# Performance work log

Hardware: AMD Instinct MI355X
Metric: run time of the kernel (lower is better)

## Reference

```python
import jax, jax.numpy as jnp
import numpy as np

D_MODEL = 2048
D_STATE = 128
D_CONV = 4
EXPAND = 2
HEADDIM = 64
NGROUPS = 1
D_INNER = EXPAND * D_MODEL            # 4096
NHEADS = D_INNER // HEADDIM           # 64
D_XBC = D_INNER + 2 * NGROUPS * D_STATE   # 4352
D_IN_PROJ = 2 * D_INNER + 2 * NGROUPS * D_STATE + NHEADS  # 8512
BLOCK_LEN = 64


def _segsum(x):
    # x: (..., T) -> (..., T, T) with segsum[i, j] = sum_{j < k <= i} x[k], -inf above diag
    T = x.shape[-1]
    xc = jnp.cumsum(x, axis=-1)
    seg = xc[..., :, None] - xc[..., None, :]
    mask = jnp.tril(jnp.ones((T, T), dtype=bool))
    return jnp.where(mask, seg, -jnp.inf)


def _ssd_scan(X, A, B, C, block_len):
    # X: (b, L, h, p), A: (b, L, h), B/C: (b, L, h, n)
    b, L, h, p = X.shape
    c = L // block_len
    X = X.reshape(b, c, block_len, h, p)
    A = A.reshape(b, c, block_len, h).transpose(0, 3, 1, 2)  # b h c l
    B = B.reshape(b, c, block_len, h, -1)
    C = C.reshape(b, c, block_len, h, -1)
    A_cumsum = jnp.cumsum(A, axis=-1)                         # b h c l
    Lmat = jnp.exp(_segsum(A))                                # b h c l l
    Y_diag = jnp.einsum('bclhn,bcshn,bhcls,bcshp->bclhp', C, B, Lmat, X)
    decay_states = jnp.exp(A_cumsum[:, :, :, -1:] - A_cumsum)  # b h c l
    states = jnp.einsum('bclhn,bhcl,bclhp->bchpn', B, decay_states, X)
    init = jnp.zeros_like(states[:, :1])
    states = jnp.concatenate([init, states], axis=1)          # b (c+1) h p n
    A_last = jnp.pad(A_cumsum[:, :, :, -1], ((0, 0), (0, 0), (1, 0)))  # b h (c+1)
    decay_chunk = jnp.exp(_segsum(A_last))                    # b h (c+1) (c+1)
    new_states = jnp.einsum('bhzc,bchpn->bzhpn', decay_chunk, states)
    states = new_states[:, 1:]                                # b c h p n
    state_decay_out = jnp.exp(A_cumsum)                       # b h c l
    Y_off = jnp.einsum('bclhn,bchpn,bhcl->bclhp', C, states, state_decay_out)
    return (Y_diag + Y_off).reshape(b, L, h, p)


def _forward(x, in_proj_w, conv_w, conv_b, A_log, D, dt_bias, norm_w, out_proj_w):
    Bsz, L, _ = x.shape
    proj = x @ in_proj_w.T                                    # (B, L, d_in_proj)
    z = proj[:, :, :D_INNER]
    xBC = proj[:, :, D_INNER:D_INNER + D_XBC]
    dt_raw = proj[:, :, D_INNER + D_XBC:]
    # depthwise causal conv1d (torch pads both sides then truncates to L == left pad only)
    xBC_t = xBC.transpose(0, 2, 1)                            # (B, C, L)
    conv = jax.lax.conv_general_dilated(
        xBC_t, conv_w, window_strides=(1,), padding=[(D_CONV - 1, 0)],
        feature_group_count=D_XBC, dimension_numbers=('NCH', 'OIH', 'NCH'))
    conv = conv + conv_b[None, :, None]
    xBC = jax.nn.silu(conv).transpose(0, 2, 1)                # (B, L, d_xBC)
    x_ssm = xBC[:, :, :D_INNER]
    B_param = xBC[:, :, D_INNER:D_INNER + NGROUPS * D_STATE]
    C_param = xBC[:, :, D_INNER + NGROUPS * D_STATE:]
    dt = jax.nn.softplus(dt_raw + dt_bias)                    # (B, L, nheads)
    A = -jnp.exp(A_log)                                       # (nheads,)
    x_heads = x_ssm.reshape(Bsz, L, NHEADS, HEADDIM)
    hpg = NHEADS // NGROUPS
    X = x_heads * dt[..., None]
    A_disc = dt * A[None, None, :]
    B_heads = jnp.repeat(B_param.reshape(Bsz, L, NGROUPS, D_STATE), hpg, axis=2)
    C_heads = jnp.repeat(C_param.reshape(Bsz, L, NGROUPS, D_STATE), hpg, axis=2)
    pad_len = (BLOCK_LEN - L % BLOCK_LEN) % BLOCK_LEN
    if pad_len > 0:
        X = jnp.pad(X, ((0, 0), (0, pad_len), (0, 0), (0, 0)))
        A_disc = jnp.pad(A_disc, ((0, 0), (0, pad_len), (0, 0)))
        B_heads = jnp.pad(B_heads, ((0, 0), (0, pad_len), (0, 0), (0, 0)))
        C_heads = jnp.pad(C_heads, ((0, 0), (0, pad_len), (0, 0), (0, 0)))
    Y = _ssd_scan(X, A_disc, B_heads, C_heads, BLOCK_LEN)[:, :L]
    Y = Y + x_heads * D[None, None, :, None]
    y = Y.reshape(Bsz, L, D_INNER)
    y = y * jax.nn.silu(z)
    rms = jnp.sqrt(jnp.mean(y * y, axis=-1, keepdims=True) + 1e-5)
    y = y / rms * norm_w
    return y @ out_proj_w.T


def setup_inputs() -> dict:
    key = jax.random.key(0)
    ks = jax.random.split(key, 8)
    x = jax.random.normal(ks[0], (2, 2048, D_MODEL), dtype=jnp.float32)
    in_proj_w = jax.random.normal(ks[1], (D_IN_PROJ, D_MODEL), dtype=jnp.float32) * 0.02
    conv_w = jax.random.normal(ks[2], (D_XBC, 1, D_CONV), dtype=jnp.float32) * 0.2
    conv_b = jnp.zeros((D_XBC,), dtype=jnp.float32)
    A_log = jnp.log(jnp.arange(1, NHEADS + 1, dtype=jnp.float32))
    D = jnp.ones((NHEADS,), dtype=jnp.float32)
    dt_bias = jax.random.normal(ks[3], (NHEADS,), dtype=jnp.float32) * 0.1
    norm_w = jnp.ones((D_INNER,), dtype=jnp.float32)
    out_proj_w = jax.random.normal(ks[4], (D_MODEL, D_INNER), dtype=jnp.float32) * 0.02
    return {"x": x, "in_proj_w": in_proj_w, "conv_w": conv_w, "conv_b": conv_b,
            "A_log": A_log, "D": D, "dt_bias": dt_bias, "norm_w": norm_w,
            "out_proj_w": out_proj_w}


def reference(x, in_proj_w, conv_w, conv_b, A_log, D, dt_bias, norm_w, out_proj_w):
    return _forward(x, in_proj_w, conv_w, conv_b, A_log, D, dt_bias, norm_w, out_proj_w)
```

## Files before the change

### kernel.cpp

```cpp
#include <hip/hip_runtime.h>
#include <cstddef>
#include <cstdint>

#define B_SZ    2
#define SEQ     2048
#define DMODEL  2048
#define DINNER  4096
#define DSTATE  128
#define NHEADS  64
#define HEADDIM 64
#define DXBC    4352
#define NPROJ   8448
#define CHUNK   64
#define NCHUNK  32
#define TOKENS  (B_SZ*SEQ)

typedef __attribute__((ext_vector_type(8))) short short8;
typedef __attribute__((ext_vector_type(4))) float floatx4;

__device__ inline float us2f(unsigned short u) {
  union { uint32_t i; float f; } c; c.i = ((uint32_t)u) << 16; return c.f;
}
__device__ inline unsigned short f2us(float f) {
  union { float f; uint32_t i; } c; c.f = f;
  uint32_t r = (c.i + 0x7fffu + ((c.i >> 16) & 1u)) >> 16;
  return (unsigned short)r;
}
__device__ inline float plo(uint32_t v) {
  union { uint32_t i; float f; } c; c.i = v << 16; return c.f;
}
__device__ inline float phi(uint32_t v) {
  union { uint32_t i; float f; } c; c.i = v & 0xffff0000u; return c.f;
}

__global__ __launch_bounds__(256) void cast_f32_bf16(
    const float* __restrict__ src, unsigned short* __restrict__ dst, int n) {
  int i = (blockIdx.x * 256 + threadIdx.x) * 4;
  if (i < n) {
    float4 v = *(const float4*)(src + i);
    ushort4 o;
    o.x = f2us(v.x); o.y = f2us(v.y); o.z = f2us(v.z); o.w = f2us(v.w);
    *(ushort4*)(dst + i) = o;
  }
}

template<int OUT_BF16>
__global__ __launch_bounds__(256, 2) void gemm_bt_p3(
    const unsigned short* __restrict__ A, const unsigned short* __restrict__ B,
    void* __restrict__ Cout, int M, int N, int K, int GM) {
  __shared__ __align__(16) unsigned short sT[3 * 12288];
  const int tid  = threadIdx.x;
  const int lane = tid & 63;
  const int wc   = tid >> 6;
  const int fr   = lane & 15;
  const int fq   = lane >> 4;

  const int nwg  = gridDim.x;
  int wgid = blockIdx.x;
  if ((nwg & 7) == 0) wgid = (wgid & 7) * (nwg >> 3) + (wgid >> 3);
  const int bm = (wgid % GM) * 128;
  const int bn = (wgid / GM) * 256;

  floatx4 acc[8][4];
  #pragma unroll
  for (int i = 0; i < 8; ++i)
    #pragma unroll
    for (int j = 0; j < 4; ++j) acc[i][j] = (floatx4){0.f, 0.f, 0.f, 0.f};

  auto stage = [&](int rb, int kb) {
    unsigned short* dst = (unsigned short*)sT + rb * 12288;
    #pragma unroll
    for (int q = 0; q < 6; ++q) {
      if (q < 2) {
        int i = q * 256 + tid;
        int row = i >> 2, slot = i & 3;
        const unsigned short* g =
            A + (size_t)(bm + row) * K + kb + 8 * (slot ^ ((row >> 1) & 3));
        __builtin_amdgcn_global_load_lds(
            (const __attribute__((address_space(1))) uint32_t*)g,
            (__attribute__((address_space(3))) uint32_t*)(dst + i * 8), 16, 0, 0);
      } else {
        int i = (q - 2) * 256 + tid;
        int row = i >> 2, slot = i & 3;
        const unsigned short* g =
            B + (size_t)(bn + row) * K + kb + 8 * (slot ^ ((row >> 1) & 3));
        __builtin_amdgcn_global_load_lds(
            (const __attribute__((address_space(1))) uint32_t*)g,
            (__attribute__((address_space(3))) uint32_t*)(dst + 4096 + i * 8), 16, 0, 0);
      }
    }
  };

  const int NH = K >> 5;
  stage(0, 0);
  stage(1, 32);
  asm volatile("s_waitcnt vmcnt(6)" ::: "memory");
  asm volatile("s_barrier" ::: "memory");

  int cb = 0, sb = 2;
  for (int h = 0; h < NH; ++h) {
    const unsigned short* buf = (const unsigned short*)sT + cb * 12288;
    if (h + 2 < NH) stage(sb, (h + 2) << 5);

    short8 af[8], bf[4];
    #pragma unroll
    for (int i = 0; i < 8; ++i) {
      int row = i * 16 + fr;
      af[i] = *(const short8*)(buf + row * 32 + 8 * (fq ^ ((row >> 1) & 3)));
    }
    #pragma unroll
    for (int j = 0; j < 4; ++j) {
      int row = wc * 64 + j * 16 + fr;
      bf[j] = *(const short8*)(buf + 4096 + row * 32 + 8 * (fq ^ ((row >> 1) & 3)));
    }
    __builtin_amdgcn_s_setprio(1);
    #pragma unroll
    for (int i = 0; i < 8; ++i)
      #pragma unroll
      for (int j = 0; j < 4; ++j)
        acc[i][j] = __builtin_amdgcn_mfma_f32_16x16x32_bf16(af[i], bf[j], acc[i][j], 0, 0, 0);
    __builtin_amdgcn_s_setprio(0);

    if (h < NH - 2) asm volatile("s_waitcnt vmcnt(6) lgkmcnt(0)" ::: "memory");
    else            asm volatile("s_waitcnt vmcnt(0) lgkmcnt(0)" ::: "memory");
    asm volatile("s_barrier" ::: "memory");
    cb = (cb == 2) ? 0 : cb + 1;
    sb = (sb == 2) ? 0 : sb + 1;
  }

  #pragma unroll
  for (int i = 0; i < 8; ++i) {
    #pragma unroll
    for (int j = 0; j < 4; ++j) {
      int col = bn + wc * 64 + j * 16 + fr;
      #pragma unroll
      for (int r = 0; r < 4; ++r) {
        int row = bm + i * 16 + fq * 4 + r;
        if (OUT_BF16)
          ((unsigned short*)Cout)[(size_t)row * N + col] = f2us(acc[i][j][r]);
        else
          ((float*)Cout)[(size_t)row * N + col] = acc[i][j][r];
      }
    }
  }
}

__device__ inline void loadA4(const float* p, float* d) {
  float4 v = *(const float4*)p; d[0]=v.x; d[1]=v.y; d[2]=v.z; d[3]=v.w;
}
__device__ inline void loadA4(const unsigned short* p, float* d) {
  ushort4 v = *(const ushort4*)p;
  d[0]=us2f(v.x); d[1]=us2f(v.y); d[2]=us2f(v.z); d[3]=us2f(v.w);
}
__device__ inline void store8(float* C, size_t off, const float* v) {
  *(float4*)(C + off)     = make_float4(v[0], v[1], v[2], v[3]);
  *(float4*)(C + off + 4) = make_float4(v[4], v[5], v[6], v[7]);
}
__device__ inline void store8(unsigned short* C, size_t off, const float* v) {
  ushort4 a; a.x=f2us(v[0]); a.y=f2us(v[1]); a.z=f2us(v[2]); a.w=f2us(v[3]);
  ushort4 b; b.x=f2us(v[4]); b.y=f2us(v[5]); b.z=f2us(v[6]); b.w=f2us(v[7]);
  *(ushort4*)(C + off) = a; *(ushort4*)(C + off + 4) = b;
}

template<typename AT, typename OT>
__global__ __launch_bounds__(256) void gemm_nt(
    const AT* __restrict__ A, const float* __restrict__ Bw,
    OT* __restrict__ C, int M, int N, int K) {
  __shared__ float As[16][128+4];
  __shared__ float Bs[16][128+4];
  const int bm = blockIdx.y * 128;
  const int bn = blockIdx.x * 128;
  const int tid = threadIdx.x;
  const int tx = tid & 15, ty = tid >> 4;

  float acc[8][8];
  #pragma unroll
  for (int i = 0; i < 8; ++i)
    #pragma unroll
    for (int j = 0; j < 8; ++j) acc[i][j] = 0.f;

  for (int k0 = 0; k0 < K; k0 += 16) {
    #pragma unroll
    for (int r = 0; r < 2; ++r) {
      int i = tid + r * 256;
      int m  = i >> 2;
      int kv = (i & 3) << 2;
      float va[4];
      loadA4(A + (size_t)(bm + m) * K + k0 + kv, va);
      As[kv+0][m] = va[0]; As[kv+1][m] = va[1]; As[kv+2][m] = va[2]; As[kv+3][m] = va[3];
      float vb[4] = {0.f, 0.f, 0.f, 0.f};
      if (bn + m < N) loadA4(Bw + (size_t)(bn + m) * K + k0 + kv, vb);
      Bs[kv+0][m] = vb[0]; Bs[kv+1][m] = vb[1]; Bs[kv+2][m] = vb[2]; Bs[kv+3][m] = vb[3];
    }
    __syncthreads();
    #pragma unroll
    for (int kk = 0; kk < 16; ++kk) {
      float ra[8], rb[8];
      *(float4*)&ra[0] = *(const float4*)&As[kk][ty*8];
      *(float4*)&ra[4] = *(const float4*)&As[kk][ty*8+4];
      *(float4*)&rb[0] = *(const float4*)&Bs[kk][tx*8];
      *(float4*)&rb[4] = *(const float4*)&Bs[kk][tx*8+4];
      #pragma unroll
      for (int i = 0; i < 8; ++i)
        #pragma unroll
        for (int j = 0; j < 8; ++j) acc[i][j] += ra[i] * rb[j];
    }
    __syncthreads();
  }
  #pragma unroll
  for (int i = 0; i < 8; ++i) {
    int m  = bm + ty*8 + i;
    int n0 = bn + tx*8;
    if (n0 < N) store8(C, (size_t)m * N + n0, &acc[i][0]);
  }
}

__global__ __launch_bounds__(256) void dt_gemm(
    const float* __restrict__ x, const float* __restrict__ W,
    float* __restrict__ dtr) {
  __shared__ float sX[32][64];
  __shared__ float sW[32][64];
  const int tid = threadIdx.x;
  const int t0 = blockIdx.x * 64;
  const int tx = tid & 15;
  const int ty = tid >> 4;
  const float* Wdt = W + (size_t)NPROJ * DMODEL;

  float acc[4][4];
  #pragma unroll
  for (int i = 0; i < 4; ++i)
    #pragma unroll
    for (int j = 0; j < 4; ++j) acc[i][j] = 0.f;

  const int r  = tid >> 3;
  const int kq = (tid & 7) * 4;

  for (int k0 = 0; k0 < DMODEL; k0 += 32) {
    __syncthreads();
    #pragma unroll
    for (int rr = 0; rr < 2; ++rr) {
      int t = r + rr * 32;
      float4 v = *(const float4*)(x + (size_t)(t0 + t) * DMODEL + k0 + kq);
      sX[kq+0][t] = v.x; sX[kq+1][t] = v.y; sX[kq+2][t] = v.z; sX[kq+3][t] = v.w;
    }
    #pragma unroll
    for (int rr = 0; rr < 2; ++rr) {
      int hh = r + rr * 32;
      float4 v = *(const float4*)(Wdt + (size_t)hh * DMODEL + k0 + kq);
      sW[kq+0][hh] = v.x; sW[kq+1][hh] = v.y; sW[kq+2][hh] = v.z; sW[kq+3][hh] = v.w;
    }
    __syncthreads();
    #pragma unroll
    for (int kk = 0; kk < 32; ++kk) {
      float4 ra = *(const float4*)&sX[kk][ty*4];
      float4 rb = *(const float4*)&sW[kk][tx*4];
      float a[4] = {ra.x, ra.y, ra.z, ra.w};
      float b[4] = {rb.x, rb.y, rb.z, rb.w};
      #pragma unroll
      for (int i = 0; i < 4; ++i)
        #pragma unroll
        for (int j = 0; j < 4; ++j)
          acc[i][j] += a[i] * b[j];
    }
  }
  #pragma unroll
  for (int i = 0; i < 4; ++i) {
    float4 o = make_float4(acc[i][0], acc[i][1], acc[i][2], acc[i][3]);
    *(float4*)(dtr + (size_t)(t0 + ty*4 + i) * NHEADS + tx*4) = o;
  }
}

__global__ __launch_bounds__(256) void bc_conv_g(
    const unsigned short* __restrict__ proj, const float* __restrict__ cw,
    const float* __restrict__ cb, unsigned short* __restrict__ bcact,
    float* __restrict__ gbuf) {
  const int c = blockIdx.x & 31;
  const int b = blockIdx.x >> 5;
  const int tid = threadIdx.x;
  const int t0 = b * SEQ + c * CHUNK;
  __shared__ unsigned short sB[64*130];
  __shared__ unsigned short sC[64*130];
  for (int i = tid; i < 64*256; i += 256) {
    int s = i >> 8, ch = i & 255;
    int cx = 4096 + ch;
    int lb = c * CHUNK + s;
    float acc = cb[cx];
    #pragma unroll
    for (int j = 0; j < 4; ++j) {
      int ll = lb - 3 + j;
      if (ll >= 0)
        acc += cw[cx*4 + j] * us2f(proj[(size_t)(b*SEQ + ll) * NPROJ + DINNER + cx]);
    }
    float v = acc / (1.f + expf(-acc));
    unsigned short uv = f2us(v);
    if (ch < 128) sB[s*130 + ch] = uv;
    else          sC[s*130 + (ch - 128)] = uv;
    bcact[(size_t)(t0 + s) * 256 + ch] = uv;
  }
  __syncthreads();
  const int l = tid >> 2, q = tid & 3;
  float g[16];
  #pragma unroll
  for (int j = 0; j < 16; ++j) g[j] = 0.f;
  const uint32_t* Cu = (const uint32_t*)&sC[l * 130];
  for (int u = 0; u < 64; ++u) {
    uint32_t cv = Cu[u];
    float c0 = plo(cv), c1 = phi(cv);
    #pragma unroll
    for (int j = 0; j < 16; ++j) {
      uint32_t bv = ((const uint32_t*)&sB[(q*16 + j) * 130])[u];
      g[j] += c0 * plo(bv) + c1 * phi(bv);
    }
  }
  float* gr = gbuf + ((size_t)(b*NCHUNK + c)) * 4096 + l*64 + q*16;
  #pragma unroll
  for (int j = 0; j < 16; ++j) gr[j] = g[j];
}

__global__ __launch_bounds__(256, 4) void ssd_phase_a2_mfma(
    const unsigned short* __restrict__ proj, const unsigned short* __restrict__ bcact,
    const float* __restrict__ dtr, const float* __restrict__ cw,
    const float* __restrict__ cb, const float* __restrict__ A_log,
    const float* __restrict__ dt_bias, const float* __restrict__ gbuf,
    const float* __restrict__ Dv,
    unsigned short* __restrict__ cs, float* __restrict__ acs,
    unsigned short* __restrict__ yscan) {
  const int h = blockIdx.x & 63;
  const int c = (blockIdx.x >> 6) & 31;
  const int b = blockIdx.x >> 11;
  const int tid = threadIdx.x;
  const int t0 = b * SEQ + c * CHUNK;
  const int lane = tid & 63, wave = tid >> 6;
  const int fr = lane & 15, fq = lane >> 4;

  __shared__ __align__(16) unsigned short sBt[128*72];
  __shared__ __align__(16) unsigned short sXh[64*72];
  __shared__ __align__(16) unsigned short sW[64*72];
  __shared__ float sdt[64], sAc[64], sdecay[64];

  const float Ah = -expf(A_log[h]);
  if (tid < 64) {
    float raw = dtr[(size_t)(t0 + tid) * NHEADS + h] + dt_bias[h];
    float dt = (raw > 20.f) ? raw : log1pf(expf(raw));
    sdt[tid] = dt;
    float v = dt * Ah;
    #pragma unroll
    for (int off = 1; off < 64; off <<= 1) {
      float o = __shfl_up(v, off, 64);
      if (tid >= off) v += o;
    }
    sAc[tid] = v;
    float alast = __shfl(v, 63, 64);
    sdecay[tid] = expf(alast - v);
    acs[((size_t)((b*NHEADS + h)*NCHUNK + c))*64 + tid] = v;
  }
  __syncthreads();
  for (int i = tid; i < 64*128; i += 256) {
    int s = i >> 7, n = i & 127;
    float v = us2f(bcact[(size_t)(t0 + s) * 256 + n]) * sdt[s] * sdecay[s];
    sBt[n*72 + s] = f2us(v);
  }
  for (int i = tid; i < 64*64; i += 256) {
    int s = i >> 6, p = i & 63;
    int cx = h * HEADDIM + p;
    int lb = c * CHUNK + s;
    float acc = cb[cx];
    #pragma unroll
    for (int j = 0; j < 4; ++j) {
      int ll = lb - 3 + j;
      if (ll >= 0)
        acc += cw[cx*4 + j] * us2f(proj[(size_t)(b*SEQ + ll) * NPROJ + DINNER + cx]);
    }
    float xh = acc / (1.f + expf(-acc));
    sXh[p*72 + s] = f2us(xh);
  }
  {
    const float* gr = gbuf + ((size_t)(b*NCHUNK + c)) * 4096;
    for (int i = tid; i < 4096; i += 256) {
      int l = i >> 6, s = i & 63;
      float w = (s <= l) ? gr[i] * expf(sAc[l] - sAc[s]) * sdt[s] : 0.f;
      sW[l*72 + s] = f2us(w);
    }
  }
  __syncthreads();

  floatx4 accy[4];
  #pragma unroll
  for (int j = 0; j < 4; ++j) accy[j] = (floatx4){0.f, 0.f, 0.f, 0.f};
  #pragma unroll
  for (int k0 = 0; k0 < 64; k0 += 32) {
    short8 af = *(const short8*)(sW + (wave*16 + fr)*72 + k0 + fq*8);
    #pragma unroll
    for (int j = 0; j < 4; ++j) {
      short8 bf = *(const short8*)(sXh + (j*16 + fr)*72 + k0 + fq*8);
      accy[j] = __builtin_amdgcn_mfma_f32_16x16x32_bf16(af, bf, accy[j], 0, 0, 0);
    }
  }
  const float Dh = Dv[h];
  #pragma unroll
  for (int j = 0; j < 4; ++j) {
    int p = j*16 + fr;
    #pragma unroll
    for (int r = 0; r < 4; ++r) {
      int l = wave*16 + fq*4 + r;
      float yd = accy[j][r] + us2f(sXh[p*72 + l]) * Dh;
      yscan[(size_t)(t0 + l) * DINNER + h*HEADDIM + p] = f2us(yd);
    }
  }
  floatx4 accs[8];
  #pragma unroll
  for (int j = 0; j < 8; ++j) accs[j] = (floatx4){0.f, 0.f, 0.f, 0.f};
  #pragma unroll
  for (int k0 = 0; k0 < 64; k0 += 32) {
    short8 af = *(const short8*)(sXh + (wave*16 + fr)*72 + k0 + fq*8);
    #pragma unroll
    for (int j = 0; j < 8; ++j) {
      short8 bf = *(const short8*)(sBt + (j*16 + fr)*72 + k0 + fq*8);
      accs[j] = __builtin_amdgcn_mfma_f32_16x16x32_bf16(af, bf, accs[j], 0, 0, 0);
    }
  }
  const size_t csb = ((size_t)((b*NHEADS + h)*NCHUNK + c)) * (HEADDIM*DSTATE);
  #pragma unroll
  for (int j = 0; j < 8; ++j) {
    int n = j*16 + fr;
    #pragma unroll
    for (int r = 0; r < 4; ++r) {
      int p = wave*16 + fq*4 + r;
      cs[csb + p*128 + n] = f2us(accs[j][r]);
    }
  }
}

__global__ __launch_bounds__(256) void ssd_scan_states(
    unsigned short* __restrict__ cs, const float* __restrict__ acs) {
  int idx = blockIdx.x * 256 + threadIdx.x;
  int e  = idx & 8191;
  int bh = idx >> 13;
  float S = 0.f;
  for (int c = 0; c < NCHUNK; ++c) {
    float al = acs[((size_t)bh*NCHUNK + c)*64 + 63];
    size_t o = ((size_t)bh*NCHUNK + c)*(HEADDIM*DSTATE) + e;
    S = S * expf(al) + us2f(cs[o]);
    cs[o] = f2us(S);
  }
}

__global__ __launch_bounds__(256, 4) void ssd_phase_c_mfma(
    const unsigned short* __restrict__ bcact, const unsigned short* __restrict__ cs,
    const float* __restrict__ acs, unsigned short* __restrict__ yscan) {
  const int h = blockIdx.x & 63;
  const int c = (blockIdx.x >> 6) & 31;
  const int b = blockIdx.x >> 11;
  const int tid = threadIdx.x;
  const int t0 = b * SEQ + c * CHUNK;
  const int lane = tid & 63, wave = tid >> 6;
  const int fr = lane & 15, fq = lane >> 4;

  __shared__ __align__(16) unsigned short sC[64*136];
  __shared__ __align__(16) unsigned short sS[64*136];
  __shared__ float seAc[64];

  const size_t csb = ((size_t)((b*NHEADS + h)*NCHUNK + c)) * (HEADDIM*DSTATE);
  for (int i = tid; i < 8192; i += 256) {
    int p = i >> 7, n = i & 127;
    sS[p*136 + n] = cs[csb + i];
  }
  for (int i = tid; i < 8192; i += 256) {
    int l = i >> 7, n = i & 127;
    sC[l*136 + n] = bcact[(size_t)(t0 + l) * 256 + 128 + n];
  }
  if (tid < 64) seAc[tid] = expf(acs[((size_t)((b*NHEADS + h)*NCHUNK + c))*64 + tid]);
  __syncthreads();

  floatx4 acc[4];
  #pragma unroll
  for (int j = 0; j < 4; ++j) acc[j] = (floatx4){0.f, 0.f, 0.f, 0.f};
  #pragma unroll
  for (int k0 = 0; k0 < 128; k0 += 32) {
    short8 af = *(const short8*)(sC + (wave*16 + fr)*136 + k0 + fq*8);
    #pragma unroll
    for (int j = 0; j < 4; ++j) {
      short8 bf = *(const short8*)(sS + (j*16 + fr)*136 + k0 + fq*8);
      acc[j] = __builtin_amdgcn_mfma_f32_16x16x32_bf16(af, bf, acc[j], 0, 0, 0);
    }
  }
  #pragma unroll
  for (int j = 0; j < 4; ++j) {
    int p = j*16 + fr;
    #pragma unroll
    for (int r = 0; r < 4; ++r) {
      int l = wave*16 + fq*4 + r;
      size_t yi = (size_t)(t0 + l) * DINNER + h*HEADDIM + p;
      yscan[yi] = f2us(us2f(yscan[yi]) + acc[j][r] * seAc[l]);
    }
  }
}

__global__ __launch_bounds__(256) void gate_rmsnorm2(
    const unsigned short* __restrict__ proj, const float* __restrict__ norm_w,
    unsigned short* __restrict__ yscan) {
  const int t = blockIdx.x;
  const int tid = threadIdx.x;
  __shared__ float ybuf[DINNER];
  __shared__ float wpart[4];
  __shared__ float sinv;
  float ss = 0.f;
  for (int i = tid; i < DINNER; i += 256) {
    float zv = us2f(proj[(size_t)t * NPROJ + i]);
    float yv = us2f(yscan[(size_t)t * DINNER + i]) * (zv / (1.f + expf(-zv)));
    ybuf[i] = yv;
    ss += yv * yv;
  }
  #pragma unroll
  for (int off = 32; off > 0; off >>= 1) ss += __shfl_down(ss, off, 64);
  if ((tid & 63) == 0) wpart[tid >> 6] = ss;
  __syncthreads();
  if (tid == 0) {
    float tot = wpart[0] + wpart[1] + wpart[2] + wpart[3];
    sinv = 1.f / sqrtf(tot / (float)DINNER + 1e-5f);
  }
  __syncthreads();
  float inv = sinv;
  for (int i = tid; i < DINNER; i += 256)
    yscan[(size_t)t * DINNER + i] = f2us(ybuf[i] * inv * norm_w[i]);
}

__global__ __launch_bounds__(512) void ssd_fused(
    const unsigned short* __restrict__ proj, const float* __restrict__ dtr,
    const float* __restrict__ cw, const float* __restrict__ cb,
    const float* __restrict__ A_log, const float* __restrict__ dt_bias,
    unsigned short* __restrict__ yscan) {
  const int h = blockIdx.x & 63;
  const int b = blockIdx.x >> 6;
  const int tid = threadIdx.x;

  __shared__ unsigned short sB[64*130];
  __shared__ unsigned short sC[64*130];
  __shared__ unsigned short sX[64*66];
  __shared__ float sW[64*65];
  __shared__ float sdt[64], sAc[64], sdecay[64], seAc[64];

  const float Ah = -expf(A_log[h]);
  const float dbias = dt_bias[h];

  float S[16];
  #pragma unroll
  for (int j = 0; j < 16; ++j) S[j] = 0.f;

  const int lG  = tid >> 3;
  const int oc  = tid & 7;

  for (int c = 0; c < NCHUNK; ++c) {
    const int t0 = b * SEQ + c * CHUNK;
    __syncthreads();
    if (tid < 64) {
      float raw = dtr[(size_t)(t0 + tid) * NHEADS + h] + dbias;
      sdt[tid] = (raw > 20.f) ? raw : log1pf(expf(raw));
    }
    for (int i = tid; i < 64*256; i += 512) {
      int s = i >> 8, ch = i & 255;
      int cx = 4096 + ch;
      int lb = c * CHUNK + s;
      float acc = cb[cx];
      #pragma unroll
      for (int j = 0; j < 4; ++j) {
        int ll = lb - 3 + j;
        if (ll >= 0)
          acc += cw[cx*4 + j] * us2f(proj[(size_t)(b*SEQ + ll) * NPROJ + DINNER + cx]);
      }
      float v = acc / (1.f + expf(-acc));
      if (ch < 128) sB[s*130 + ch] = f2us(v);
      else          sC[s*130 + (ch - 128)] = f2us(v);
    }
    __syncthreads();
    if (tid == 0) {
      float run = 0.f;
      for (int s = 0; s < CHUNK; ++s) { run += sdt[s] * Ah; sAc[s] = run; }
    }
    __syncthreads();
    if (tid < 64) {
      float last = sAc[63];
      sdecay[tid] = expf(last - sAc[tid]);
      seAc[tid]   = expf(sAc[tid]);
    }
    for (int i = tid; i < 64*64; i += 512) {
      int s = i >> 6, p = i & 63;
      int cx = h * HEADDIM + p;
      int lb = c * CHUNK + s;
      float acc = cb[cx];
      #pragma unroll
      for (int j = 0; j < 4; ++j) {
        int ll = lb - 3 + j;
        if (ll >= 0)
          acc += cw[cx*4 + j] * us2f(proj[(size_t)(b*SEQ + ll) * NPROJ + DINNER + cx]);
      }
      float v = acc / (1.f + expf(-acc));
      sX[s*66 + p] = f2us(v * sdt[s]);
    }
    __syncthreads();

    float g[8];
    #pragma unroll
    for (int j = 0; j < 8; ++j) g[j] = 0.f;
    {
      const uint32_t* Cu = (const uint32_t*)&sC[lG * 130];
      for (int u = 0; u < 64; ++u) {
        uint32_t cv = Cu[u];
        float c0 = plo(cv), c1 = phi(cv);
        #pragma unroll
        for (int j = 0; j < 8; ++j) {
          uint32_t bv = ((const uint32_t*)&sB[(oc*8 + j) * 130])[u];
          g[j] += c0 * plo(bv) + c1 * phi(bv);
        }
      }
    }
    {
      float acl = sAc[lG];
      #pragma unroll
      for (int j = 0; j < 8; ++j) {
        int s = oc*8 + j;
        sW[lG*65 + s] = (s <= lG) ? g[j] * expf(acl - sAc[s]) : 0.f;
      }
    }
    {
      float elast = expf(sAc[63]);
      #pragma unroll
      for (int j = 0; j < 16; ++j) S[j] *= elast;
      for (int s = 0; s < CHUNK; ++s) {
        float w = sdecay[s] * us2f(sX[s*66 + lG]);
        const uint32_t* Bu = (const uint32_t*)&sB[s*130 + oc*16];
        #pragma unroll
        for (int ju = 0; ju < 8; ++ju) {
          uint32_t bv = Bu[ju];
          S[2*ju]   += plo(bv) * w;
          S[2*ju+1] += phi(bv) * w;
        }
      }
    }
    __syncthreads();
    #pragma unroll
    for (int j = 0; j < 16; ++j) sB[lG*130 + oc*16 + j] = f2us(S[j]);
    __syncthreads();
    for (int o = tid; o < CHUNK*HEADDIM; o += 512) {
      int l = o >> 6, p = o & 63;
      float yd = 0.f;
      for (int s = 0; s <= l; ++s)
        yd += sW[l*65 + s] * us2f(sX[s*66 + p]);
      float yo = 0.f;
      const uint32_t* Cu = (const uint32_t*)&sC[l * 130];
      const uint32_t* Su = (const uint32_t*)&sB[p * 130];
      for (int u = 0; u < 64; ++u) {
        uint32_t cv = Cu[u], sv = Su[u];
        yo += plo(cv) * plo(sv) + phi(cv) * phi(sv);
      }
      float y = yd + yo * seAc[l];
      yscan[(size_t)(t0 + l) * DINNER + h * HEADDIM + p] = f2us(y);
    }
  }
}

__global__ __launch_bounds__(256) void gate_rmsnorm_dskip(
    const unsigned short* __restrict__ proj, const float* __restrict__ cw,
    const float* __restrict__ cb, const float* __restrict__ Dv,
    const float* __restrict__ norm_w, unsigned short* __restrict__ yscan) {
  const int t = blockIdx.x;
  const int tid = threadIdx.x;
  const int b = t >> 11, lb = t & 2047;
  __shared__ float ybuf[DINNER];
  __shared__ float wpart[4];
  __shared__ float sinv;
  float ss = 0.f;
  for (int i = tid; i < DINNER; i += 256) {
    float zv = us2f(proj[(size_t)t * NPROJ + i]);
    float acc = cb[i];
    #pragma unroll
    for (int j = 0; j < 4; ++j) {
      int ll = lb - 3 + j;
      if (ll >= 0)
        acc += cw[i*4 + j] * us2f(proj[(size_t)(b*SEQ + ll) * NPROJ + DINNER + i]);
    }
    float xh = acc / (1.f + expf(-acc));
    float yv = us2f(yscan[(size_t)t * DINNER + i]) + xh * Dv[i >> 6];
    yv = yv * (zv / (1.f + expf(-zv)));
    ybuf[i] = yv;
    ss += yv * yv;
  }
  #pragma unroll
  for (int off = 32; off > 0; off >>= 1) ss += __shfl_down(ss, off, 64);
  if ((tid & 63) == 0) wpart[tid >> 6] = ss;
  __syncthreads();
  if (tid == 0) {
    float tot = wpart[0] + wpart[1] + wpart[2] + wpart[3];
    sinv = 1.f / sqrtf(tot / (float)DINNER + 1e-5f);
  }
  __syncthreads();
  float inv = sinv;
  for (int i = tid; i < DINNER; i += 256)
    yscan[(size_t)t * DINNER + i] = f2us(ybuf[i] * inv * norm_w[i]);
}

extern "C" void kernel_launch(void* const* d_in, const int* in_sizes, int n_in,
                              void* d_out, int out_size, void* d_ws, size_t ws_size,
                              hipStream_t stream) {
  const float* x          = (const float*)d_in[0];
  const float* in_proj_w  = (const float*)d_in[1];
  const float* conv_w     = (const float*)d_in[2];
  const float* conv_b     = (const float*)d_in[3];
  const float* A_log      = (const float*)d_in[4];
  const float* Dv         = (const float*)d_in[5];
  const float* dt_bias    = (const float*)d_in[6];
  const float* norm_w     = (const float*)d_in[7];
  const float* out_proj_w = (const float*)d_in[8];
  float* out = (float*)d_out;

  unsigned short* proj  = (unsigned short*)d_ws;
  float*          dtr   = (float*)(proj + (size_t)TOKENS * NPROJ);
  unsigned short* yscan = (unsigned short*)(dtr + (size_t)TOKENS * NHEADS);
  unsigned short* cs    = yscan + (size_t)TOKENS * DINNER;
  float*          acs   = (float*)(cs + (size_t)B_SZ*NHEADS*NCHUNK*HEADDIM*DSTATE);
  unsigned short* bcact = (unsigned short*)(acs + (size_t)B_SZ*NHEADS*NCHUNK*64);
  float*          gbuf  = (float*)(bcact + (size_t)TOKENS*256);
  const size_t NEEDED = (size_t)((char*)(gbuf + (size_t)B_SZ*NCHUNK*4096) - (char*)d_ws);

  unsigned short* xb  = cs;
  unsigned short* wib = xb + (size_t)TOKENS * DMODEL;
  unsigned short* wob = proj;

  if (ws_size >= NEEDED) {
    cast_f32_bf16<<<(TOKENS*DMODEL)/1024, 256, 0, stream>>>(x, xb, TOKENS*DMODEL);
    cast_f32_bf16<<<((size_t)NPROJ*DMODEL)/1024, 256, 0, stream>>>(in_proj_w, wib, NPROJ*DMODEL);
    {
      int nwg = (TOKENS/128) * (NPROJ/256);
      gemm_bt_p3<1><<<nwg, 256, 0, stream>>>(xb, wib, proj, TOKENS, NPROJ, DMODEL, TOKENS/128);
    }
    dt_gemm<<<TOKENS/64, 256, 0, stream>>>(x, in_proj_w, dtr);
    bc_conv_g<<<B_SZ*NCHUNK, 256, 0, stream>>>(proj, conv_w, conv_b, bcact, gbuf);
    ssd_phase_a2_mfma<<<B_SZ*NCHUNK*NHEADS, 256, 0, stream>>>(
        proj, bcact, dtr, conv_w, conv_b, A_log, dt_bias, gbuf, Dv, cs, acs, yscan);
    ssd_scan_states<<<(B_SZ*NHEADS*HEADDIM*DSTATE)/256, 256, 0, stream>>>(cs, acs);
    ssd_phase_c_mfma<<<B_SZ*NCHUNK*NHEADS, 256, 0, stream>>>(bcact, cs, acs, yscan);
    gate_rmsnorm2<<<TOKENS, 256, 0, stream>>>(proj, norm_w, yscan);
    cast_f32_bf16<<<((size_t)DMODEL*DINNER)/1024, 256, 0, stream>>>(out_proj_w, wob, DMODEL*DINNER);
    {
      int nwg = (TOKENS/128) * (DMODEL/256);
      gemm_bt_p3<0><<<nwg, 256, 0, stream>>>(yscan, wob, out, TOKENS, DMODEL, DINNER, TOKENS/128);
    }
  } else {
    {
      dim3 grid(NPROJ/128, TOKENS/128);
      gemm_nt<float, unsigned short><<<grid, 256, 0, stream>>>(
          x, in_proj_w, proj, TOKENS, NPROJ, DMODEL);
    }
    dt_gemm<<<TOKENS/64, 256, 0, stream>>>(x, in_proj_w, dtr);
    ssd_fused<<<B_SZ*NHEADS, 512, 0, stream>>>(proj, dtr, conv_w, conv_b,
                                               A_log, dt_bias, yscan);
    gate_rmsnorm_dskip<<<TOKENS, 256, 0, stream>>>(proj, conv_w, conv_b, Dv, norm_w, yscan);
    {
      dim3 grid(DMODEL/128, TOKENS/128);
      gemm_nt<unsigned short, float><<<grid, 256, 0, stream>>>(
          yscan, out_proj_w, out, TOKENS, DMODEL, DINNER);
    }
  }
}
```

Before: 796.0 us.

## Vectorize SSD helper kernels and use 64-row tiles for out-projection GEMM

Templates the bf16 GEMM on the M tile size and runs the out-projection with 64-row tiles, doubling the workgroup count for the small N=2048 GEMM. The conv, scan, chunk and gate/rmsnorm kernels now stage conv inputs in LDS, read them once, and use 16-byte vector loads and stores instead of scalar ones. The state scan now has each thread handle eight elements. Phase A's occupancy hint is lowered from 4 to 3 blocks to fit the extra LDS. These changes target memory inefficiency and low parallelism in the auxiliary kernels, at the cost of more LDS use and register pressure.

```diff
diff --git a/kernel.cpp b/kernel.cpp
--- a/kernel.cpp
+++ b/kernel.cpp
@@ -44,11 +44,16 @@
   }
 }
 
-template<int OUT_BF16>
+template<int OUT_BF16, int BMT>
 __global__ __launch_bounds__(256, 2) void gemm_bt_p3(
     const unsigned short* __restrict__ A, const unsigned short* __restrict__ B,
     void* __restrict__ Cout, int M, int N, int K, int GM) {
-  __shared__ __align__(16) unsigned short sT[3 * 12288];
+  constexpr int ACH   = BMT / 64;
+  constexpr int NCH   = ACH + 4;
+  constexpr int ABASE = ACH * 2048;
+  constexpr int BUFS  = (BMT + 256) * 32;
+  constexpr int NI    = BMT / 16;
+  __shared__ __align__(16) unsigned short sT[3 * BUFS];
   const int tid  = threadIdx.x;
   const int lane = tid & 63;
   const int wc   = tid >> 6;
@@ -58,20 +63,20 @@
   const int nwg  = gridDim.x;
   int wgid = blockIdx.x;
   if ((nwg & 7) == 0) wgid = (wgid & 7) * (nwg >> 3) + (wgid >> 3);
-  const int bm = (wgid % GM) * 128;
+  const int bm = (wgid % GM) * BMT;
   const int bn = (wgid / GM) * 256;
 
-  floatx4 acc[8][4];
-  #pragma unroll
-  for (int i = 0; i < 8; ++i)
+  floatx4 acc[NI][4];
+  #pragma unroll
+  for (int i = 0; i < NI; ++i)
     #pragma unroll
     for (int j = 0; j < 4; ++j) acc[i][j] = (floatx4){0.f, 0.f, 0.f, 0.f};
 
   auto stage = [&](int rb, int kb) {
-    unsigned short* dst = (unsigned short*)sT + rb * 12288;
-    #pragma unroll
-    for (int q = 0; q < 6; ++q) {
-      if (q < 2) {
+    unsigned short* dst = (unsigned short*)sT + rb * BUFS;
+    #pragma unroll
+    for (int q = 0; q < NCH; ++q) {
+      if (q < ACH) {
         int i = q * 256 + tid;
         int row = i >> 2, slot = i & 3;
         const unsigned short* g =
@@ -80,13 +85,13 @@
             (const __attribute__((address_space(1))) uint32_t*)g,
             (__attribute__((address_space(3))) uint32_t*)(dst + i * 8), 16, 0, 0);
       } else {
-        int i = (q - 2) * 256 + tid;
+        int i = (q - ACH) * 256 + tid;
         int row = i >> 2, slot = i & 3;
         const unsigned short* g =
             B + (size_t)(bn + row) * K + kb + 8 * (slot ^ ((row >> 1) & 3));
         __builtin_amdgcn_global_load_lds(
             (const __attribute__((address_space(1))) uint32_t*)g,
-            (__attribute__((address_space(3))) uint32_t*)(dst + 4096 + i * 8), 16, 0, 0);
+            (__attribute__((address_space(3))) uint32_t*)(dst + ABASE + i * 8), 16, 0, 0);
       }
     }
   };
@@ -94,42 +99,47 @@
   const int NH = K >> 5;
   stage(0, 0);
   stage(1, 32);
-  asm volatile("s_waitcnt vmcnt(6)" ::: "memory");
+  if constexpr (NCH == 6) asm volatile("s_waitcnt vmcnt(6)" ::: "memory");
+  else                    asm volatile("s_waitcnt vmcnt(5)" ::: "memory");
   asm volatile("s_barrier" ::: "memory");
 
   int cb = 0, sb = 2;
   for (int h = 0; h < NH; ++h) {
-    const unsigned short* buf = (const unsigned short*)sT + cb * 12288;
+    const unsigned short* buf = (const unsigned short*)sT + cb * BUFS;
     if (h + 2 < NH) stage(sb, (h + 2) << 5);
 
-    short8 af[8], bf[4];
-    #pragma unroll
-    for (int i = 0; i < 8; ++i) {
+    short8 af[NI], bf[4];
+    #pragma unroll
+    for (int i = 0; i < NI; ++i) {
       int row = i * 16 + fr;
       af[i] = *(const short8*)(buf + row * 32 + 8 * (fq ^ ((row >> 1) & 3)));
     }
     #pragma unroll
     for (int j = 0; j < 4; ++j) {
       int row = wc * 64 + j * 16 + fr;
-      bf[j] = *(const short8*)(buf + 4096 + row * 32 + 8 * (fq ^ ((row >> 1) & 3)));
+      bf[j] = *(const short8*)(buf + ABASE + row * 32 + 8 * (fq ^ ((row >> 1) & 3)));
     }
     __builtin_amdgcn_s_setprio(1);
     #pragma unroll
-    for (int i = 0; i < 8; ++i)
+    for (int i = 0; i < NI; ++i)
       #pragma unroll
       for (int j = 0; j < 4; ++j)
         acc[i][j] = __builtin_amdgcn_mfma_f32_16x16x32_bf16(af[i], bf[j], acc[i][j], 0, 0, 0);
     __builtin_amdgcn_s_setprio(0);
 
-    if (h < NH - 2) asm volatile("s_waitcnt vmcnt(6) lgkmcnt(0)" ::: "memory");
-    else            asm volatile("s_waitcnt vmcnt(0) lgkmcnt(0)" ::: "memory");
+    if (h < NH - 2) {
+      if constexpr (NCH == 6) asm volatile("s_waitcnt vmcnt(6) lgkmcnt(0)" ::: "memory");
+      else                    asm volatile("s_waitcnt vmcnt(5) lgkmcnt(0)" ::: "memory");
+    } else {
+      asm volatile("s_waitcnt vmcnt(0) lgkmcnt(0)" ::: "memory");
+    }
     asm volatile("s_barrier" ::: "memory");
     cb = (cb == 2) ? 0 : cb + 1;
     sb = (sb == 2) ? 0 : sb + 1;
   }
 
   #pragma unroll
-  for (int i = 0; i < 8; ++i) {
+  for (int i = 0; i < NI; ++i) {
     #pragma unroll
     for (int j = 0; j < 4; ++j) {
       int col = bn + wc * 64 + j * 16 + fr;
@@ -278,46 +288,70 @@
   const int b = blockIdx.x >> 5;
   const int tid = threadIdx.x;
   const int t0 = b * SEQ + c * CHUNK;
-  __shared__ unsigned short sB[64*130];
-  __shared__ unsigned short sC[64*130];
-  for (int i = tid; i < 64*256; i += 256) {
-    int s = i >> 8, ch = i & 255;
-    int cx = 4096 + ch;
-    int lb = c * CHUNK + s;
-    float acc = cb[cx];
-    #pragma unroll
-    for (int j = 0; j < 4; ++j) {
-      int ll = lb - 3 + j;
-      if (ll >= 0)
-        acc += cw[cx*4 + j] * us2f(proj[(size_t)(b*SEQ + ll) * NPROJ + DINNER + cx]);
-    }
-    float v = acc / (1.f + expf(-acc));
-    unsigned short uv = f2us(v);
-    if (ch < 128) sB[s*130 + ch] = uv;
-    else          sC[s*130 + (ch - 128)] = uv;
-    bcact[(size_t)(t0 + s) * 256 + ch] = uv;
+  __shared__ __align__(16) unsigned short sIn[67 * 256];
+  __shared__ __align__(16) unsigned short sB[64 * 136];
+  __shared__ __align__(16) unsigned short sC[64 * 136];
+  __shared__ float scw[256 * 4];
+  __shared__ float scb[256];
+
+  *(float4*)&scw[tid * 4] = *(const float4*)(cw + (size_t)(4096 + tid) * 4);
+  scb[tid] = cb[4096 + tid];
+
+  for (int i = tid; i < 67 * 32; i += 256) {
+    int r = i >> 5, ch0 = (i & 31) * 8;
+    int ll = c * CHUNK - 3 + r;
+    short8 v = {0,0,0,0,0,0,0,0};
+    if (ll >= 0)
+      v = *(const short8*)(proj + (size_t)(b * SEQ + ll) * NPROJ + 8192 + ch0);
+    *(short8*)&sIn[r * 256 + ch0] = v;
   }
   __syncthreads();
+
+  for (int i = tid; i < 64 * 32; i += 256) {
+    int s = i >> 5, ch0 = (i & 31) * 8;
+    short8 i0 = *(const short8*)&sIn[(s + 0) * 256 + ch0];
+    short8 i1 = *(const short8*)&sIn[(s + 1) * 256 + ch0];
+    short8 i2 = *(const short8*)&sIn[(s + 2) * 256 + ch0];
+    short8 i3 = *(const short8*)&sIn[(s + 3) * 256 + ch0];
+    short8 o;
+    #pragma unroll
+    for (int e = 0; e < 8; ++e) {
+      int ch = ch0 + e;
+      float a = scb[ch]
+        + scw[ch*4+0] * us2f((unsigned short)i0[e])
+        + scw[ch*4+1] * us2f((unsigned short)i1[e])
+        + scw[ch*4+2] * us2f((unsigned short)i2[e])
+        + scw[ch*4+3] * us2f((unsigned short)i3[e]);
+      float v = a / (1.f + expf(-a));
+      o[e] = (short)f2us(v);
+    }
+    if (ch0 < 128) *(short8*)&sB[s * 136 + ch0] = o;
+    else           *(short8*)&sC[s * 136 + (ch0 - 128)] = o;
+    *(short8*)(bcact + (size_t)(t0 + s) * 256 + ch0) = o;
+  }
+  __syncthreads();
+
   const int l = tid >> 2, q = tid & 3;
   float g[16];
   #pragma unroll
   for (int j = 0; j < 16; ++j) g[j] = 0.f;
-  const uint32_t* Cu = (const uint32_t*)&sC[l * 130];
+  const uint32_t* Cu = (const uint32_t*)&sC[l * 136];
   for (int u = 0; u < 64; ++u) {
     uint32_t cv = Cu[u];
     float c0 = plo(cv), c1 = phi(cv);
     #pragma unroll
     for (int j = 0; j < 16; ++j) {
-      uint32_t bv = ((const uint32_t*)&sB[(q*16 + j) * 130])[u];
+      uint32_t bv = ((const uint32_t*)&sB[(q*16 + j) * 136])[u];
       g[j] += c0 * plo(bv) + c1 * phi(bv);
     }
   }
   float* gr = gbuf + ((size_t)(b*NCHUNK + c)) * 4096 + l*64 + q*16;
   #pragma unroll
-  for (int j = 0; j < 16; ++j) gr[j] = g[j];
-}
-
-__global__ __launch_bounds__(256, 4) void ssd_phase_a2_mfma(
+  for (int j = 0; j < 4; ++j)
+    *(float4*)(gr + j*4) = make_float4(g[j*4], g[j*4+1], g[j*4+2], g[j*4+3]);
+}
+
+__global__ __launch_bounds__(256, 3) void ssd_phase_a2_mfma(
     const unsigned short* __restrict__ proj, const unsigned short* __restrict__ bcact,
     const float* __restrict__ dtr, const float* __restrict__ cw,
     const float* __restrict__ cb, const float* __restrict__ A_log,
@@ -333,9 +367,12 @@
   const int lane = tid & 63, wave = tid >> 6;
   const int fr = lane & 15, fq = lane >> 4;
 
+  __shared__ __align__(16) unsigned short sIn[67 * 64];
   __shared__ __align__(16) unsigned short sBt[128*72];
   __shared__ __align__(16) unsigned short sXh[64*72];
   __shared__ __align__(16) unsigned short sW[64*72];
+  __shared__ float cwl[64 * 4];
+  __shared__ float cbl[64];
   __shared__ float sdt[64], sAc[64], sdecay[64];
 
   const float Ah = -expf(A_log[h]);
@@ -354,32 +391,63 @@
     sdecay[tid] = expf(alast - v);
     acs[((size_t)((b*NHEADS + h)*NCHUNK + c))*64 + tid] = v;
   }
+  if (tid >= 64 && tid < 128) {
+    int p = tid - 64;
+    *(float4*)&cwl[p * 4] = *(const float4*)(cw + (size_t)(h * HEADDIM + p) * 4);
+    cbl[p] = cb[h * HEADDIM + p];
+  }
+  for (int i = tid; i < 67 * 8; i += 256) {
+    int r = i >> 3, p0 = (i & 7) * 8;
+    int ll = c * CHUNK - 3 + r;
+    short8 v = {0,0,0,0,0,0,0,0};
+    if (ll >= 0)
+      v = *(const short8*)(proj + (size_t)(b * SEQ + ll) * NPROJ + DINNER + h * HEADDIM + p0);
+    *(short8*)&sIn[r * 64 + p0] = v;
+  }
   __syncthreads();
-  for (int i = tid; i < 64*128; i += 256) {
-    int s = i >> 7, n = i & 127;
-    float v = us2f(bcact[(size_t)(t0 + s) * 256 + n]) * sdt[s] * sdecay[s];
-    sBt[n*72 + s] = f2us(v);
-  }
-  for (int i = tid; i < 64*64; i += 256) {
-    int s = i >> 6, p = i & 63;
-    int cx = h * HEADDIM + p;
-    int lb = c * CHUNK + s;
-    float acc = cb[cx];
-    #pragma unroll
-    for (int j = 0; j < 4; ++j) {
-      int ll = lb - 3 + j;
-      if (ll >= 0)
-        acc += cw[cx*4 + j] * us2f(proj[(size_t)(b*SEQ + ll) * NPROJ + DINNER + cx]);
-    }
-    float xh = acc / (1.f + expf(-acc));
-    sXh[p*72 + s] = f2us(xh);
+
+  for (int i = tid; i < 64 * 16; i += 256) {
+    int s = i >> 4, n0 = (i & 15) * 8;
+    float sc = sdt[s] * sdecay[s];
+    short8 v = *(const short8*)(bcact + (size_t)(t0 + s) * 256 + n0);
+    #pragma unroll
+    for (int e = 0; e < 8; ++e)
+      sBt[(n0 + e) * 72 + s] = f2us(us2f((unsigned short)v[e]) * sc);
+  }
+  for (int i = tid; i < 64 * 8; i += 256) {
+    int s = i >> 3, p0 = (i & 7) * 8;
+    short8 i0 = *(const short8*)&sIn[(s + 0) * 64 + p0];
+    short8 i1 = *(const short8*)&sIn[(s + 1) * 64 + p0];
+    short8 i2 = *(const short8*)&sIn[(s + 2) * 64 + p0];
+    short8 i3 = *(const short8*)&sIn[(s + 3) * 64 + p0];
+    #pragma unroll
+    for (int e = 0; e < 8; ++e) {
+      int p = p0 + e;
+      float a = cbl[p]
+        + cwl[p*4+0] * us2f((unsigned short)i0[e])
+        + cwl[p*4+1] * us2f((unsigned short)i1[e])
+        + cwl[p*4+2] * us2f((unsigned short)i2[e])
+        + cwl[p*4+3] * us2f((unsigned short)i3[e]);
+      float xh = a / (1.f + expf(-a));
+      sXh[p * 72 + s] = f2us(xh);
+    }
   }
   {
     const float* gr = gbuf + ((size_t)(b*NCHUNK + c)) * 4096;
-    for (int i = tid; i < 4096; i += 256) {
-      int l = i >> 6, s = i & 63;
-      float w = (s <= l) ? gr[i] * expf(sAc[l] - sAc[s]) * sdt[s] : 0.f;
-      sW[l*72 + s] = f2us(w);
+    for (int i = tid; i < 512; i += 256) {
+      int l = i >> 3, s0 = (i & 7) * 8;
+      float4 g0 = *(const float4*)(gr + l * 64 + s0);
+      float4 g1 = *(const float4*)(gr + l * 64 + s0 + 4);
+      float gv[8] = {g0.x, g0.y, g0.z, g0.w, g1.x, g1.y, g1.z, g1.w};
+      float acl = sAc[l];
+      short8 o;
+      #pragma unroll
+      for (int e = 0; e < 8; ++e) {
+        int s = s0 + e;
+        float w = (s <= l) ? gv[e] * expf(acl - sAc[s]) * sdt[s] : 0.f;
+        o[e] = (short)f2us(w);
+      }
+      *(short8*)&sW[l * 72 + s0] = o;
     }
   }
   __syncthreads();
@@ -434,14 +502,22 @@
 __global__ __launch_bounds__(256) void ssd_scan_states(
     unsigned short* __restrict__ cs, const float* __restrict__ acs) {
   int idx = blockIdx.x * 256 + threadIdx.x;
-  int e  = idx & 8191;
-  int bh = idx >> 13;
-  float S = 0.f;
+  int bh = idx >> 10;
+  int e0 = (idx & 1023) * 8;
+  float S[8];
+  #pragma unroll
+  for (int j = 0; j < 8; ++j) S[j] = 0.f;
   for (int c = 0; c < NCHUNK; ++c) {
-    float al = acs[((size_t)bh*NCHUNK + c)*64 + 63];
-    size_t o = ((size_t)bh*NCHUNK + c)*(HEADDIM*DSTATE) + e;
-    S = S * expf(al) + us2f(cs[o]);
-    cs[o] = f2us(S);
+    float al = expf(acs[((size_t)bh*NCHUNK + c)*64 + 63]);
+    size_t o = ((size_t)bh*NCHUNK + c)*(HEADDIM*DSTATE) + e0;
+    short8 v = *(const short8*)(cs + o);
+    short8 w;
+    #pragma unroll
+    for (int j = 0; j < 8; ++j) {
+      S[j] = S[j] * al + us2f((unsigned short)v[j]);
+      w[j] = (short)f2us(S[j]);
+    }
+    *(short8*)(cs + o) = w;
   }
 }
 
@@ -461,13 +537,14 @@
   __shared__ float seAc[64];
 
   const size_t csb = ((size_t)((b*NHEADS + h)*NCHUNK + c)) * (HEADDIM*DSTATE);
-  for (int i = tid; i < 8192; i += 256) {
-    int p = i >> 7, n = i & 127;
-    sS[p*136 + n] = cs[csb + i];
-  }
-  for (int i = tid; i < 8192; i += 256) {
-    int l = i >> 7, n = i & 127;
-    sC[l*136 + n] = bcact[(size_t)(t0 + l) * 256 + 128 + n];
+  for (int i = tid; i < 1024; i += 256) {
+    int p = i >> 4, n0 = (i & 15) * 8;
+    *(short8*)&sS[p * 136 + n0] = *(const short8*)(cs + csb + p * 128 + n0);
+  }
+  for (int i = tid; i < 1024; i += 256) {
+    int l = i >> 4, n0 = (i & 15) * 8;
+    *(short8*)&sC[l * 136 + n0] =
+        *(const short8*)(bcact + (size_t)(t0 + l) * 256 + 128 + n0);
   }
   if (tid < 64) seAc[tid] = expf(acs[((size_t)((b*NHEADS + h)*NCHUNK + c))*64 + tid]);
   __syncthreads();
@@ -501,15 +578,22 @@
     unsigned short* __restrict__ yscan) {
   const int t = blockIdx.x;
   const int tid = threadIdx.x;
-  __shared__ float ybuf[DINNER];
   __shared__ float wpart[4];
   __shared__ float sinv;
+  float yv[16];
   float ss = 0.f;
-  for (int i = tid; i < DINNER; i += 256) {
-    float zv = us2f(proj[(size_t)t * NPROJ + i]);
-    float yv = us2f(yscan[(size_t)t * DINNER + i]) * (zv / (1.f + expf(-zv)));
-    ybuf[i] = yv;
-    ss += yv * yv;
+  #pragma unroll
+  for (int g = 0; g < 2; ++g) {
+    int i = (g * 256 + tid) * 8;
+    short8 z8 = *(const short8*)(proj + (size_t)t * NPROJ + i);
+    short8 y8 = *(const short8*)(yscan + (size_t)t * DINNER + i);
+    #pragma unroll
+    for (int e = 0; e < 8; ++e) {
+      float zv = us2f((unsigned short)z8[e]);
+      float v = us2f((unsigned short)y8[e]) * (zv / (1.f + expf(-zv)));
+      yv[g*8+e] = v;
+      ss += v * v;
+    }
   }
   #pragma unroll
   for (int off = 32; off > 0; off >>= 1) ss += __shfl_down(ss, off, 64);
@@ -521,8 +605,18 @@
   }
   __syncthreads();
   float inv = sinv;
-  for (int i = tid; i < DINNER; i += 256)
-    yscan[(size_t)t * DINNER + i] = f2us(ybuf[i] * inv * norm_w[i]);
+  #pragma unroll
+  for (int g = 0; g < 2; ++g) {
+    int i = (g * 256 + tid) * 8;
+    float4 w0 = *(const float4*)(norm_w + i);
+    float4 w1 = *(const float4*)(norm_w + i + 4);
+    float wv[8] = {w0.x, w0.y, w0.z, w0.w, w1.x, w1.y, w1.z, w1.w};
+    short8 o;
+    #pragma unroll
+    for (int e = 0; e < 8; ++e)
+      o[e] = (short)f2us(yv[g*8+e] * inv * wv[e]);
+    *(short8*)(yscan + (size_t)t * DINNER + i) = o;
+  }
 }
 
 __global__ __launch_bounds__(512) void ssd_fused(
@@ -731,19 +825,19 @@
     cast_f32_bf16<<<((size_t)NPROJ*DMODEL)/1024, 256, 0, stream>>>(in_proj_w, wib, NPROJ*DMODEL);
     {
       int nwg = (TOKENS/128) * (NPROJ/256);
-      gemm_bt_p3<1><<<nwg, 256, 0, stream>>>(xb, wib, proj, TOKENS, NPROJ, DMODEL, TOKENS/128);
+      gemm_bt_p3<1,128><<<nwg, 256, 0, stream>>>(xb, wib, proj, TOKENS, NPROJ, DMODEL, TOKENS/128);
     }
     dt_gemm<<<TOKENS/64, 256, 0, stream>>>(x, in_proj_w, dtr);
     bc_conv_g<<<B_SZ*NCHUNK, 256, 0, stream>>>(proj, conv_w, conv_b, bcact, gbuf);
     ssd_phase_a2_mfma<<<B_SZ*NCHUNK*NHEADS, 256, 0, stream>>>(
         proj, bcact, dtr, conv_w, conv_b, A_log, dt_bias, gbuf, Dv, cs, acs, yscan);
-    ssd_scan_states<<<(B_SZ*NHEADS*HEADDIM*DSTATE)/256, 256, 0, stream>>>(cs, acs);
+    ssd_scan_states<<<(B_SZ*NHEADS*HEADDIM*DSTATE)/(256*8), 256, 0, stream>>>(cs, acs);
     ssd_phase_c_mfma<<<B_SZ*NCHUNK*NHEADS, 256, 0, stream>>>(bcact, cs, acs, yscan);
     gate_rmsnorm2<<<TOKENS, 256, 0, stream>>>(proj, norm_w, yscan);
     cast_f32_bf16<<<((size_t)DMODEL*DINNER)/1024, 256, 0, stream>>>(out_proj_w, wob, DMODEL*DINNER);
     {
-      int nwg = (TOKENS/128) * (DMODEL/256);
-      gemm_bt_p3<0><<<nwg, 256, 0, stream>>>(yscan, wob, out, TOKENS, DMODEL, DINNER, TOKENS/128);
+      int nwg = (TOKENS/64) * (DMODEL/256);
+      gemm_bt_p3<0,64><<<nwg, 256, 0, stream>>>(yscan, wob, out, TOKENS, DMODEL, DINNER, TOKENS/64);
     }
   } else {
     {
```

After: 702.8 us. 11.7% less time.
